# Performance work log

Hardware: AMD Instinct MI355X
Metric: run time of the kernel (lower is better)

The kernel has to match this reference:

```python
import jax, jax.numpy as jnp
import numpy as np

GROUP_SIZE = 128
LORA_SCALING = 32.0 / 16.0  # lora_alpha / r


def _unpack_rows(q):
    # q: int32 [n, m] -> uint4 values [n*8, m], 8 nibbles per int32 along axis 0
    shifts = (jnp.arange(8, dtype=jnp.int32) * 4)
    vals = (q[:, None, :] >> shifts[None, :, None]) & 0xF
    return vals.reshape(q.shape[0] * 8, q.shape[1])


def _unpack_cols(q):
    # q: int32 [g, m] -> uint4 values [g, m*8], 8 nibbles per int32 along axis 1
    shifts = (jnp.arange(8, dtype=jnp.int32) * 4)
    vals = (q[:, :, None] >> shifts[None, None, :]) & 0xF
    return vals.reshape(q.shape[0], q.shape[1] * 8)


def setup_inputs() -> dict:
    key = jax.random.key(0)
    ks = jax.random.split(key, 6)
    in_f, out_f, tokens, r = 4096, 11008, 64, 16
    g = in_f // GROUP_SIZE  # 32 groups
    x = jax.random.normal(ks[0], (tokens, in_f), dtype=jnp.float32)
    qweight = jax.random.randint(ks[1], (in_f // 8, out_f), jnp.iinfo(jnp.int32).min, jnp.iinfo(jnp.int32).max, dtype=jnp.int32)
    qzeros = jax.random.randint(ks[2], (g, out_f // 8), jnp.iinfo(jnp.int32).min, jnp.iinfo(jnp.int32).max, dtype=jnp.int32)
    scales = jax.random.uniform(ks[3], (g, out_f), dtype=jnp.float32) * 0.01 + 0.001
    lora_A = jax.random.normal(ks[4], (r, in_f), dtype=jnp.float32) * 0.02
    lora_B = jax.random.normal(ks[5], (out_f, r), dtype=jnp.float32) * 0.02
    return {"x": x, "qweight": qweight, "qzeros": qzeros, "scales": scales,
            "lora_A": lora_A, "lora_B": lora_B}


def reference(x, qweight, qzeros, scales, lora_A, lora_B):
    in_f = qweight.shape[0] * 8
    # --- GPTQ int4 dequant ---
    wq = _unpack_rows(qweight).astype(jnp.float32)          # [in, out]
    zeros = (_unpack_cols(qzeros) + 1).astype(jnp.float32)  # [groups, out] (GPTQ +1 offset)
    g_idx = jnp.arange(in_f) // GROUP_SIZE                  # [in]
    W = scales[g_idx] * (wq - zeros[g_idx])                 # [in, out]
    # base quantized matmul
    result = x @ W                                          # [tokens, out]
    # --- LoRA adapter (single active adapter, dropout=0, tmp_weight=1) ---
    lora_out = (x @ lora_A.T) @ lora_B.T                    # [tokens, out]
    return result + lora_out * LORA_SCALING
```

## Files before the change

kernel.cpp:

```cpp
#include <hip/hip_runtime.h>
#include <stdint.h>

#define TOKENS 64
#define IN_F   4096
#define OUT_F  11008
#define RANK   16
#define GS     128
#define NG     32
#define ZCOLS  (OUT_F / 8)
#define LORA_SCALE 2.0f

using short8  = __attribute__((ext_vector_type(8))) short;
using float4v = __attribute__((ext_vector_type(4))) float;

static __device__ inline uint16_t f2bf(float f, float* back) {
    uint32_t u = __float_as_uint(f);
    uint32_t r = (u + 0x7FFFu + ((u >> 16) & 1u)) >> 16;
    *back = __uint_as_float(r << 16);
    return (uint16_t)r;
}

__global__ __launch_bounds__(256) void prep_kernel(
        const float* __restrict__ x,
        const float* __restrict__ loraA,
        uint4* __restrict__ xf4,
        float* __restrict__ xsumT,
        float* __restrict__ midT) {
    __shared__ float redg[256];
    __shared__ float redm[4][16];
    const int t    = blockIdx.x;
    const int tid  = threadIdx.x;
    const int lane = tid & 63;
    const int wv   = tid >> 6;

    float4 xv[4];
    const float4* xp = (const float4*)(x + (size_t)t * IN_F + tid * 16);
    #pragma unroll
    for (int i = 0; i < 4; ++i) xv[i] = xp[i];

    union { uint16_t u[16]; uint4 q[2]; } ob;
    float s = 0.f;
    #pragma unroll
    for (int i = 0; i < 4; ++i) {
        float b;
        ob.u[i * 4 + 0] = f2bf(xv[i].x, &b); s += b;
        ob.u[i * 4 + 1] = f2bf(xv[i].y, &b); s += b;
        ob.u[i * 4 + 2] = f2bf(xv[i].z, &b); s += b;
        ob.u[i * 4 + 3] = f2bf(xv[i].w, &b); s += b;
    }
    {
        const int mm = t >> 4, nn = t & 15;
        const int kchunk = tid >> 1;
        #pragma unroll
        for (int i = 0; i < 2; ++i) {
            const int qd = (tid * 2 + i) & 3;
            xf4[(size_t)((mm * 128 + kchunk) * 64 + qd * 16 + nn)] = ob.q[i];
        }
    }
    redg[tid] = s;

    float pj[16];
    #pragma unroll
    for (int j = 0; j < 16; ++j) {
        const float4* ap = (const float4*)(loraA + (size_t)j * IN_F + tid * 16);
        float ps = 0.f;
        #pragma unroll
        for (int i = 0; i < 4; ++i) {
            float4 a = ap[i];
            ps += a.x * xv[i].x + a.y * xv[i].y + a.z * xv[i].z + a.w * xv[i].w;
        }
        pj[j] = ps;
    }
    #pragma unroll
    for (int j = 0; j < 16; ++j) {
        #pragma unroll
        for (int off = 32; off; off >>= 1) pj[j] += __shfl_down(pj[j], off);
    }
    if (lane == 0) {
        #pragma unroll
        for (int j = 0; j < 16; ++j) redm[wv][j] = pj[j];
    }
    __syncthreads();
    if (tid < NG) {
        float g = 0.f;
        #pragma unroll
        for (int i = 0; i < 8; ++i) g += redg[tid * 8 + i];
        xsumT[tid * TOKENS + t] = g;
    }
    if (tid < 16)
        midT[tid * TOKENS + t] = redm[0][tid] + redm[1][tid] + redm[2][tid] + redm[3][tid];
}

__global__ __launch_bounds__(256) void lora_out_kernel(
        const float* __restrict__ midT,
        const float* __restrict__ loraB,
        float* __restrict__ out) {
    const int gid = blockIdx.x * 256 + threadIdx.x;
    const int t = gid / OUT_F;
    const int o = gid - t * OUT_F;
    const float4* b4 = (const float4*)(loraB + (size_t)o * RANK);
    float s = 0.f;
    #pragma unroll
    for (int i = 0; i < 4; ++i) {
        float4 b = b4[i];
        s += b.x * midT[(i * 4 + 0) * TOKENS + t];
        s += b.y * midT[(i * 4 + 1) * TOKENS + t];
        s += b.z * midT[(i * 4 + 2) * TOKENS + t];
        s += b.w * midT[(i * 4 + 3) * TOKENS + t];
    }
    out[gid] = s * LORA_SCALE;
}

#define LOADG(st, g) do {                                                       \
    _Pragma("unroll")                                                           \
    for (int mt = 0; mt < 2; ++mt)                                              \
        _Pragma("unroll")                                                       \
        for (int ks = 0; ks < 4; ++ks)                                          \
            A[st][mt * 4 + ks] =                                                \
                xf4[(size_t)(((mh * 2 + mt) * 128 + (g) * 4 + ks) * 64) + lane];\
    _Pragma("unroll")                                                           \
    for (int ks = 0; ks < 4; ++ks)                                              \
        _Pragma("unroll")                                                       \
        for (int nh = 0; nh < 2; ++nh)                                          \
            B[st][ks * 2 + nh] =                                                \
                qwc[(size_t)((g) * 16 + ks * 4 + quad) * OUT_F + nh * 16];      \
    _Pragma("unroll")                                                           \
    for (int mt = 0; mt < 2; ++mt)                                              \
        XS[st][mt] = *(const float4*)(xsumT + (g) * 64 +                        \
                                      (mh * 2 + mt) * 16 + quad * 4);           \
    _Pragma("unroll")                                                           \
    for (int nh = 0; nh < 2; ++nh) {                                            \
        S[st][nh] = scales[(size_t)(g) * OUT_F + col0 + nh * 16 + n];           \
        Z[st][nh] = qz[(size_t)(g) * ZCOLS + ((col0 + nh * 16 + n) >> 3)];      \
    }                                                                           \
} while (0)

#define COMPUTEG(st) do {                                                       \
    float4v accg[2][2];                                                         \
    _Pragma("unroll")                                                           \
    for (int mt = 0; mt < 2; ++mt)                                              \
        _Pragma("unroll")                                                       \
        for (int nh = 0; nh < 2; ++nh)                                          \
            accg[mt][nh] = (float4v){0.f, 0.f, 0.f, 0.f};                       \
    _Pragma("unroll")                                                           \
    for (int ks = 0; ks < 4; ++ks) {                                            \
        union { uint4 u; short8 s; } af0, af1;                                  \
        af0.u = A[st][ks];                                                      \
        af1.u = A[st][4 + ks];                                                  \
        _Pragma("unroll")                                                       \
        for (int nh = 0; nh < 2; ++nh) {                                        \
            uint32_t q  = B[st][ks * 2 + nh];                                   \
            uint32_t lo = q & 0x0F0F0F0Fu;                                      \
            uint32_t hi = (q >> 4) & 0x0F0F0F0Fu;                               \
            union { uint32_t u32[4]; short8 s8; } bf;                           \
            _Pragma("unroll")                                                   \
            for (int i = 0; i < 4; ++i)                                         \
                bf.u32[i] = __builtin_amdgcn_perm(hi, lo,                       \
                                0x0C040C00u + i * 0x00010001u) | 0x43004300u;   \
            accg[0][nh] = __builtin_amdgcn_mfma_f32_16x16x32_bf16(af0.s, bf.s8, \
                                                            accg[0][nh], 0, 0, 0);\
            accg[1][nh] = __builtin_amdgcn_mfma_f32_16x16x32_bf16(af1.s, bf.s8, \
                                                            accg[1][nh], 0, 0, 0);\
        }                                                                       \
    }                                                                           \
    _Pragma("unroll")                                                           \
    for (int nh = 0; nh < 2; ++nh) {                                            \
        const float zoff = (float)(((Z[st][nh] >>                               \
                        (((col0 + nh * 16 + n) & 7) * 4)) & 0xFu) + 129u);      \
        const float scl = S[st][nh];                                            \
        _Pragma("unroll")                                                       \
        for (int mt = 0; mt < 2; ++mt) {                                        \
            const float xr[4] = {XS[st][mt].x, XS[st][mt].y,                    \
                                 XS[st][mt].z, XS[st][mt].w};                   \
            _Pragma("unroll")                                                   \
            for (int r = 0; r < 4; ++r)                                         \
                acc[mt][nh][r] = fmaf(scl, fmaf(-zoff, xr[r],                   \
                                      accg[mt][nh][r]), acc[mt][nh][r]);        \
        }                                                                       \
    }                                                                           \
} while (0)

__global__ __launch_bounds__(256, 3) void main_kernel(
        const uint32_t* __restrict__ qw,
        const uint32_t* __restrict__ qz,
        const float* __restrict__ scales,
        const uint4* __restrict__ xf4,
        const float* __restrict__ xsumT,
        float* __restrict__ out) {
    const int tid  = threadIdx.x;
    const int wv   = tid >> 6;
    const int lane = tid & 63;
    const int n    = lane & 15;
    const int quad = lane >> 4;
    const int mh   = wv & 1;
    const int cs   = wv >> 1;
    const int colblk = blockIdx.x >> 2;
    const int kseg   = blockIdx.x & 3;
    const int col0   = colblk * 64 + cs * 32;
    const int g0     = kseg * 8;

    const uint32_t* qwc = qw + col0 + n;

    float4v acc[2][2];
    #pragma unroll
    for (int mt = 0; mt < 2; ++mt)
        #pragma unroll
        for (int nh = 0; nh < 2; ++nh)
            acc[mt][nh] = (float4v){0.f, 0.f, 0.f, 0.f};

    uint4    A[2][8];
    uint32_t B[2][8];
    float4   XS[2][2];
    float    S[2][2];
    uint32_t Z[2][2];

    LOADG(0, g0);
    LOADG(1, g0 + 1);
    #pragma unroll
    for (int gi = 0; gi < 8; ++gi) {
        const int st = gi & 1;
        COMPUTEG(st);
        int gl = gi + 2; if (gl > 7) gl = 7;
        LOADG(st, g0 + gl);
    }

    #pragma unroll
    for (int mt = 0; mt < 2; ++mt)
        #pragma unroll
        for (int nh = 0; nh < 2; ++nh)
            #pragma unroll
            for (int r = 0; r < 4; ++r) {
                const int t = (mh * 2 + mt) * 16 + quad * 4 + r;
                atomicAdd(out + (size_t)t * OUT_F + col0 + nh * 16 + n,
                          acc[mt][nh][r]);
            }
}

extern "C" void kernel_launch(void* const* d_in, const int* in_sizes, int n_in,
                              void* d_out, int out_size, void* d_ws, size_t ws_size,
                              hipStream_t stream) {
    const float*    x      = (const float*)d_in[0];
    const uint32_t* qw     = (const uint32_t*)d_in[1];
    const uint32_t* qz     = (const uint32_t*)d_in[2];
    const float*    scales = (const float*)d_in[3];
    const float*    loraA  = (const float*)d_in[4];
    const float*    loraB  = (const float*)d_in[5];
    float* out = (float*)d_out;

    uint4* xf4   = (uint4*)d_ws;
    float* xsumT = (float*)((char*)d_ws + (size_t)TOKENS * IN_F * 2);
    float* midT  = xsumT + NG * TOKENS;

    prep_kernel<<<TOKENS, 256, 0, stream>>>(x, loraA, xf4, xsumT, midT);
    lora_out_kernel<<<(TOKENS * OUT_F) / 256, 256, 0, stream>>>(midT, loraB, out);
    main_kernel<<<(OUT_F / 64) * 4, 256, 0, stream>>>(qw, qz, scales, xf4, xsumT, out);
}
```

Baseline: 106.9 us.

## Fuse LoRA output into main GEMM and drop split-K atomics

```diff
diff --git a/kernel.cpp b/kernel.cpp
--- a/kernel.cpp
+++ b/kernel.cpp
@@ -20,12 +20,16 @@
     return (uint16_t)r;
 }
 
+static __device__ inline float dot4(float4 a, float4 b) {
+    return a.x * b.x + a.y * b.y + a.z * b.z + a.w * b.w;
+}
+
 __global__ __launch_bounds__(256) void prep_kernel(
         const float* __restrict__ x,
         const float* __restrict__ loraA,
         uint4* __restrict__ xf4,
         float* __restrict__ xsumT,
-        float* __restrict__ midT) {
+        float* __restrict__ midTT) {
     __shared__ float redg[256];
     __shared__ float redm[4][16];
     const int t    = blockIdx.x;
@@ -88,27 +92,7 @@
         xsumT[tid * TOKENS + t] = g;
     }
     if (tid < 16)
-        midT[tid * TOKENS + t] = redm[0][tid] + redm[1][tid] + redm[2][tid] + redm[3][tid];
-}
-
-__global__ __launch_bounds__(256) void lora_out_kernel(
-        const float* __restrict__ midT,
-        const float* __restrict__ loraB,
-        float* __restrict__ out) {
-    const int gid = blockIdx.x * 256 + threadIdx.x;
-    const int t = gid / OUT_F;
-    const int o = gid - t * OUT_F;
-    const float4* b4 = (const float4*)(loraB + (size_t)o * RANK);
-    float s = 0.f;
-    #pragma unroll
-    for (int i = 0; i < 4; ++i) {
-        float4 b = b4[i];
-        s += b.x * midT[(i * 4 + 0) * TOKENS + t];
-        s += b.y * midT[(i * 4 + 1) * TOKENS + t];
-        s += b.z * midT[(i * 4 + 2) * TOKENS + t];
-        s += b.w * midT[(i * 4 + 3) * TOKENS + t];
-    }
-    out[gid] = s * LORA_SCALE;
+        midTT[t * RANK + tid] = redm[0][tid] + redm[1][tid] + redm[2][tid] + redm[3][tid];
 }
 
 #define LOADG(st, g) do {                                                       \
@@ -120,72 +104,60 @@
                 xf4[(size_t)(((mh * 2 + mt) * 128 + (g) * 4 + ks) * 64) + lane];\
     _Pragma("unroll")                                                           \
     for (int ks = 0; ks < 4; ++ks)                                              \
-        _Pragma("unroll")                                                       \
-        for (int nh = 0; nh < 2; ++nh)                                          \
-            B[st][ks * 2 + nh] =                                                \
-                qwc[(size_t)((g) * 16 + ks * 4 + quad) * OUT_F + nh * 16];      \
+        B[st][ks] = qwc[(size_t)((g) * 16 + ks * 4 + quad) * OUT_F];            \
     _Pragma("unroll")                                                           \
     for (int mt = 0; mt < 2; ++mt)                                              \
         XS[st][mt] = *(const float4*)(xsumT + (g) * 64 +                        \
                                       (mh * 2 + mt) * 16 + quad * 4);           \
-    _Pragma("unroll")                                                           \
-    for (int nh = 0; nh < 2; ++nh) {                                            \
-        S[st][nh] = scales[(size_t)(g) * OUT_F + col0 + nh * 16 + n];           \
-        Z[st][nh] = qz[(size_t)(g) * ZCOLS + ((col0 + nh * 16 + n) >> 3)];      \
-    }                                                                           \
+    S[st] = scales[(size_t)(g) * OUT_F + col];                                  \
+    Z[st] = qz[(size_t)(g) * ZCOLS + (col >> 3)];                               \
 } while (0)
 
 #define COMPUTEG(st) do {                                                       \
-    float4v accg[2][2];                                                         \
-    _Pragma("unroll")                                                           \
-    for (int mt = 0; mt < 2; ++mt)                                              \
-        _Pragma("unroll")                                                       \
-        for (int nh = 0; nh < 2; ++nh)                                          \
-            accg[mt][nh] = (float4v){0.f, 0.f, 0.f, 0.f};                       \
+    float4v accg[2];                                                            \
+    accg[0] = (float4v){0.f, 0.f, 0.f, 0.f};                                    \
+    accg[1] = (float4v){0.f, 0.f, 0.f, 0.f};                                    \
     _Pragma("unroll")                                                           \
     for (int ks = 0; ks < 4; ++ks) {                                            \
         union { uint4 u; short8 s; } af0, af1;                                  \
         af0.u = A[st][ks];                                                      \
         af1.u = A[st][4 + ks];                                                  \
+        uint32_t q  = B[st][ks];                                                \
+        uint32_t lo = q & 0x0F0F0F0Fu;                                          \
+        uint32_t hi = (q >> 4) & 0x0F0F0F0Fu;                                   \
+        union { uint32_t u32[4]; short8 s8; } bf;                               \
         _Pragma("unroll")                                                       \
-        for (int nh = 0; nh < 2; ++nh) {                                        \
-            uint32_t q  = B[st][ks * 2 + nh];                                   \
-            uint32_t lo = q & 0x0F0F0F0Fu;                                      \
-            uint32_t hi = (q >> 4) & 0x0F0F0F0Fu;                               \
-            union { uint32_t u32[4]; short8 s8; } bf;                           \
-            _Pragma("unroll")                                                   \
-            for (int i = 0; i < 4; ++i)                                         \
-                bf.u32[i] = __builtin_amdgcn_perm(hi, lo,                       \
-                                0x0C040C00u + i * 0x00010001u) | 0x43004300u;   \
-            accg[0][nh] = __builtin_amdgcn_mfma_f32_16x16x32_bf16(af0.s, bf.s8, \
-                                                            accg[0][nh], 0, 0, 0);\
-            accg[1][nh] = __builtin_amdgcn_mfma_f32_16x16x32_bf16(af1.s, bf.s8, \
-                                                            accg[1][nh], 0, 0, 0);\
-        }                                                                       \
+        for (int i = 0; i < 4; ++i)                                             \
+            bf.u32[i] = __builtin_amdgcn_perm(hi, lo,                           \
+                            0x0C040C00u + i * 0x00010001u) | 0x43004300u;       \
+        accg[0] = __builtin_amdgcn_mfma_f32_16x16x32_bf16(af0.s, bf.s8,         \
+                                                          accg[0], 0, 0, 0);    \
+        accg[1] = __builtin_amdgcn_mfma_f32_16x16x32_bf16(af1.s, bf.s8,         \
+                                                          accg[1], 0, 0, 0);    \
     }                                                                           \
-    _Pragma("unroll")                                                           \
-    for (int nh = 0; nh < 2; ++nh) {                                            \
-        const float zoff = (float)(((Z[st][nh] >>                               \
-                        (((col0 + nh * 16 + n) & 7) * 4)) & 0xFu) + 129u);      \
-        const float scl = S[st][nh];                                            \
+    {                                                                           \
+        const float zoff = (float)(((Z[st] >> ((col & 7) * 4)) & 0xFu) + 129u); \
+        const float scl = S[st];                                                \
         _Pragma("unroll")                                                       \
         for (int mt = 0; mt < 2; ++mt) {                                        \
             const float xr[4] = {XS[st][mt].x, XS[st][mt].y,                    \
                                  XS[st][mt].z, XS[st][mt].w};                   \
             _Pragma("unroll")                                                   \
             for (int r = 0; r < 4; ++r)                                         \
-                acc[mt][nh][r] = fmaf(scl, fmaf(-zoff, xr[r],                   \
-                                      accg[mt][nh][r]), acc[mt][nh][r]);        \
+                acc[mt][r] = fmaf(scl, fmaf(-zoff, xr[r],                       \
+                                  accg[mt][r]), acc[mt][r]);                    \
         }                                                                       \
     }                                                                           \
 } while (0)
 
-__global__ __launch_bounds__(256, 3) void main_kernel(
+__global__ __launch_bounds__(256) void main_kernel(
         const uint32_t* __restrict__ qw,
         const uint32_t* __restrict__ qz,
         const float* __restrict__ scales,
         const uint4* __restrict__ xf4,
         const float* __restrict__ xsumT,
+        const float* __restrict__ midTT,
+        const float* __restrict__ loraB,
         float* __restrict__ out) {
     const int tid  = threadIdx.x;
     const int wv   = tid >> 6;
@@ -194,46 +166,44 @@
     const int quad = lane >> 4;
     const int mh   = wv & 1;
     const int cs   = wv >> 1;
-    const int colblk = blockIdx.x >> 2;
-    const int kseg   = blockIdx.x & 3;
-    const int col0   = colblk * 64 + cs * 32;
-    const int g0     = kseg * 8;
-
-    const uint32_t* qwc = qw + col0 + n;
-
-    float4v acc[2][2];
-    #pragma unroll
-    for (int mt = 0; mt < 2; ++mt)
-        #pragma unroll
-        for (int nh = 0; nh < 2; ++nh)
-            acc[mt][nh] = (float4v){0.f, 0.f, 0.f, 0.f};
+    const int col  = blockIdx.x * 32 + cs * 16 + n;
+
+    const uint32_t* qwc = qw + col;
+
+    float4v acc[2];
+    acc[0] = (float4v){0.f, 0.f, 0.f, 0.f};
+    acc[1] = (float4v){0.f, 0.f, 0.f, 0.f};
 
     uint4    A[2][8];
-    uint32_t B[2][8];
+    uint32_t B[2][4];
     float4   XS[2][2];
-    float    S[2][2];
-    uint32_t Z[2][2];
-
-    LOADG(0, g0);
-    LOADG(1, g0 + 1);
-    #pragma unroll
-    for (int gi = 0; gi < 8; ++gi) {
-        const int st = gi & 1;
+    float    S[2];
+    uint32_t Z[2];
+
+    LOADG(0, 0);
+    LOADG(1, 1);
+    #pragma unroll 2
+    for (int g = 0; g < NG - 2; ++g) {
+        const int st = g & 1;
         COMPUTEG(st);
-        int gl = gi + 2; if (gl > 7) gl = 7;
-        LOADG(st, g0 + gl);
-    }
-
-    #pragma unroll
-    for (int mt = 0; mt < 2; ++mt)
-        #pragma unroll
-        for (int nh = 0; nh < 2; ++nh)
-            #pragma unroll
-            for (int r = 0; r < 4; ++r) {
-                const int t = (mh * 2 + mt) * 16 + quad * 4 + r;
-                atomicAdd(out + (size_t)t * OUT_F + col0 + nh * 16 + n,
-                          acc[mt][nh][r]);
-            }
+        LOADG(st, g + 2);
+    }
+    COMPUTEG((NG - 2) & 1);
+    COMPUTEG((NG - 1) & 1);
+
+    const float4* b4 = (const float4*)(loraB + (size_t)col * RANK);
+    const float4 b0 = b4[0], b1 = b4[1], b2 = b4[2], b3 = b4[3];
+    #pragma unroll
+    for (int mt = 0; mt < 2; ++mt) {
+        #pragma unroll
+        for (int r = 0; r < 4; ++r) {
+            const int t = (mh * 2 + mt) * 16 + quad * 4 + r;
+            const float4* m4 = (const float4*)(midTT + t * RANK);
+            const float l = dot4(b0, m4[0]) + dot4(b1, m4[1]) +
+                            dot4(b2, m4[2]) + dot4(b3, m4[3]);
+            out[(size_t)t * OUT_F + col] = acc[mt][r] + LORA_SCALE * l;
+        }
+    }
 }
 
 extern "C" void kernel_launch(void* const* d_in, const int* in_sizes, int n_in,
@@ -249,9 +219,9 @@
 
     uint4* xf4   = (uint4*)d_ws;
     float* xsumT = (float*)((char*)d_ws + (size_t)TOKENS * IN_F * 2);
-    float* midT  = xsumT + NG * TOKENS;
-
-    prep_kernel<<<TOKENS, 256, 0, stream>>>(x, loraA, xf4, xsumT, midT);
-    lora_out_kernel<<<(TOKENS * OUT_F) / 256, 256, 0, stream>>>(midT, loraB, out);
-    main_kernel<<<(OUT_F / 64) * 4, 256, 0, stream>>>(qw, qz, scales, xf4, xsumT, out);
-}
+    float* midTT = xsumT + NG * TOKENS;
+
+    prep_kernel<<<TOKENS, 256, 0, stream>>>(x, loraA, xf4, xsumT, midTT);
+    main_kernel<<<OUT_F / 32, 256, 0, stream>>>(qw, qz, scales, xf4, xsumT,
+                                                midTT, loraB, out);
+}
```

New measurement: 113.4 us. +6.1%, slower.

## Stage quantized weights through LDS with direct global-to-LDS double-buffered loads

Applied to the files above, without the earlier changes.

```diff
diff --git a/kernel.cpp b/kernel.cpp
--- a/kernel.cpp
+++ b/kernel.cpp
@@ -12,6 +12,9 @@
 
 using short8  = __attribute__((ext_vector_type(8))) short;
 using float4v = __attribute__((ext_vector_type(4))) float;
+
+typedef __attribute__((address_space(3))) uint32_t       lds_u32_t;
+typedef __attribute__((address_space(1))) const uint32_t glb_u32_t;
 
 static __device__ inline uint16_t f2bf(float f, float* back) {
     uint32_t u = __float_as_uint(f);
@@ -111,82 +114,14 @@
     out[gid] = s * LORA_SCALE;
 }
 
-#define LOADG(st, g) do {                                                       \
-    _Pragma("unroll")                                                           \
-    for (int mt = 0; mt < 2; ++mt)                                              \
-        _Pragma("unroll")                                                       \
-        for (int ks = 0; ks < 4; ++ks)                                          \
-            A[st][mt * 4 + ks] =                                                \
-                xf4[(size_t)(((mh * 2 + mt) * 128 + (g) * 4 + ks) * 64) + lane];\
-    _Pragma("unroll")                                                           \
-    for (int ks = 0; ks < 4; ++ks)                                              \
-        _Pragma("unroll")                                                       \
-        for (int nh = 0; nh < 2; ++nh)                                          \
-            B[st][ks * 2 + nh] =                                                \
-                qwc[(size_t)((g) * 16 + ks * 4 + quad) * OUT_F + nh * 16];      \
-    _Pragma("unroll")                                                           \
-    for (int mt = 0; mt < 2; ++mt)                                              \
-        XS[st][mt] = *(const float4*)(xsumT + (g) * 64 +                        \
-                                      (mh * 2 + mt) * 16 + quad * 4);           \
-    _Pragma("unroll")                                                           \
-    for (int nh = 0; nh < 2; ++nh) {                                            \
-        S[st][nh] = scales[(size_t)(g) * OUT_F + col0 + nh * 16 + n];           \
-        Z[st][nh] = qz[(size_t)(g) * ZCOLS + ((col0 + nh * 16 + n) >> 3)];      \
-    }                                                                           \
-} while (0)
-
-#define COMPUTEG(st) do {                                                       \
-    float4v accg[2][2];                                                         \
-    _Pragma("unroll")                                                           \
-    for (int mt = 0; mt < 2; ++mt)                                              \
-        _Pragma("unroll")                                                       \
-        for (int nh = 0; nh < 2; ++nh)                                          \
-            accg[mt][nh] = (float4v){0.f, 0.f, 0.f, 0.f};                       \
-    _Pragma("unroll")                                                           \
-    for (int ks = 0; ks < 4; ++ks) {                                            \
-        union { uint4 u; short8 s; } af0, af1;                                  \
-        af0.u = A[st][ks];                                                      \
-        af1.u = A[st][4 + ks];                                                  \
-        _Pragma("unroll")                                                       \
-        for (int nh = 0; nh < 2; ++nh) {                                        \
-            uint32_t q  = B[st][ks * 2 + nh];                                   \
-            uint32_t lo = q & 0x0F0F0F0Fu;                                      \
-            uint32_t hi = (q >> 4) & 0x0F0F0F0Fu;                               \
-            union { uint32_t u32[4]; short8 s8; } bf;                           \
-            _Pragma("unroll")                                                   \
-            for (int i = 0; i < 4; ++i)                                         \
-                bf.u32[i] = __builtin_amdgcn_perm(hi, lo,                       \
-                                0x0C040C00u + i * 0x00010001u) | 0x43004300u;   \
-            accg[0][nh] = __builtin_amdgcn_mfma_f32_16x16x32_bf16(af0.s, bf.s8, \
-                                                            accg[0][nh], 0, 0, 0);\
-            accg[1][nh] = __builtin_amdgcn_mfma_f32_16x16x32_bf16(af1.s, bf.s8, \
-                                                            accg[1][nh], 0, 0, 0);\
-        }                                                                       \
-    }                                                                           \
-    _Pragma("unroll")                                                           \
-    for (int nh = 0; nh < 2; ++nh) {                                            \
-        const float zoff = (float)(((Z[st][nh] >>                               \
-                        (((col0 + nh * 16 + n) & 7) * 4)) & 0xFu) + 129u);      \
-        const float scl = S[st][nh];                                            \
-        _Pragma("unroll")                                                       \
-        for (int mt = 0; mt < 2; ++mt) {                                        \
-            const float xr[4] = {XS[st][mt].x, XS[st][mt].y,                    \
-                                 XS[st][mt].z, XS[st][mt].w};                   \
-            _Pragma("unroll")                                                   \
-            for (int r = 0; r < 4; ++r)                                         \
-                acc[mt][nh][r] = fmaf(scl, fmaf(-zoff, xr[r],                   \
-                                      accg[mt][nh][r]), acc[mt][nh][r]);        \
-        }                                                                       \
-    }                                                                           \
-} while (0)
-
-__global__ __launch_bounds__(256, 3) void main_kernel(
+__global__ __launch_bounds__(256, 2) void main_kernel(
         const uint32_t* __restrict__ qw,
         const uint32_t* __restrict__ qz,
         const float* __restrict__ scales,
         const uint4* __restrict__ xf4,
         const float* __restrict__ xsumT,
         float* __restrict__ out) {
+    __shared__ uint32_t bq[2][16 * 64];
     const int tid  = threadIdx.x;
     const int wv   = tid >> 6;
     const int lane = tid & 63;
@@ -196,10 +131,13 @@
     const int cs   = wv >> 1;
     const int colblk = blockIdx.x >> 2;
     const int kseg   = blockIdx.x & 3;
-    const int col0   = colblk * 64 + cs * 32;
-    const int g0     = kseg * 8;
-
-    const uint32_t* qwc = qw + col0 + n;
+    const int blkcol0 = colblk * 64;
+    const int col0    = blkcol0 + cs * 32;
+    const int g0      = kseg * 8;
+
+    const uint32_t* qsrc = qw + (size_t)(g0 * 16 + (tid >> 4)) * OUT_F
+                              + blkcol0 + (tid & 15) * 4;
+    const size_t gstride = (size_t)16 * OUT_F;
 
     float4v acc[2][2];
     #pragma unroll
@@ -208,20 +146,89 @@
         for (int nh = 0; nh < 2; ++nh)
             acc[mt][nh] = (float4v){0.f, 0.f, 0.f, 0.f};
 
-    uint4    A[2][8];
-    uint32_t B[2][8];
-    float4   XS[2][2];
-    float    S[2][2];
-    uint32_t Z[2][2];
-
-    LOADG(0, g0);
-    LOADG(1, g0 + 1);
+    __builtin_amdgcn_global_load_lds((glb_u32_t*)qsrc,
+                                     (lds_u32_t*)&bq[0][wv * 256], 16, 0, 0);
+    __syncthreads();
+
     #pragma unroll
     for (int gi = 0; gi < 8; ++gi) {
-        const int st = gi & 1;
-        COMPUTEG(st);
-        int gl = gi + 2; if (gl > 7) gl = 7;
-        LOADG(st, g0 + gl);
+        const int cur = gi & 1;
+        const int g   = g0 + gi;
+
+        uint4 A[8];
+        #pragma unroll
+        for (int mt = 0; mt < 2; ++mt)
+            #pragma unroll
+            for (int ks = 0; ks < 4; ++ks)
+                A[mt * 4 + ks] =
+                    xf4[(size_t)(((mh * 2 + mt) * 128 + g * 4 + ks) * 64) + lane];
+        float4 XS[2];
+        #pragma unroll
+        for (int mt = 0; mt < 2; ++mt)
+            XS[mt] = *(const float4*)(xsumT + g * 64 + (mh * 2 + mt) * 16 + quad * 4);
+        float S[2]; uint32_t Z[2];
+        #pragma unroll
+        for (int nh = 0; nh < 2; ++nh) {
+            S[nh] = scales[(size_t)g * OUT_F + col0 + nh * 16 + n];
+            Z[nh] = qz[(size_t)g * ZCOLS + ((col0 + nh * 16 + n) >> 3)];
+        }
+
+        if (gi < 7)
+            __builtin_amdgcn_global_load_lds(
+                (glb_u32_t*)(qsrc + (size_t)(gi + 1) * gstride),
+                (lds_u32_t*)&bq[cur ^ 1][wv * 256], 16, 0, 0);
+
+        uint32_t Bw[8];
+        #pragma unroll
+        for (int ks = 0; ks < 4; ++ks)
+            #pragma unroll
+            for (int nh = 0; nh < 2; ++nh)
+                Bw[ks * 2 + nh] =
+                    bq[cur][(ks * 4 + quad) * 64 + cs * 32 + nh * 16 + n];
+
+        float4v accg[2][2];
+        #pragma unroll
+        for (int mt = 0; mt < 2; ++mt)
+            #pragma unroll
+            for (int nh = 0; nh < 2; ++nh)
+                accg[mt][nh] = (float4v){0.f, 0.f, 0.f, 0.f};
+        #pragma unroll
+        for (int ks = 0; ks < 4; ++ks) {
+            union { uint4 u; short8 s; } af0, af1;
+            af0.u = A[ks];
+            af1.u = A[4 + ks];
+            #pragma unroll
+            for (int nh = 0; nh < 2; ++nh) {
+                uint32_t q  = Bw[ks * 2 + nh];
+                uint32_t lo = q & 0x0F0F0F0Fu;
+                uint32_t hi = (q >> 4) & 0x0F0F0F0Fu;
+                union { uint32_t u32[4]; short8 s8; } bf;
+                #pragma unroll
+                for (int i = 0; i < 4; ++i)
+                    bf.u32[i] = __builtin_amdgcn_perm(hi, lo,
+                                    0x0C040C00u + i * 0x00010001u) | 0x43004300u;
+                accg[0][nh] = __builtin_amdgcn_mfma_f32_16x16x32_bf16(
+                                    af0.s, bf.s8, accg[0][nh], 0, 0, 0);
+                accg[1][nh] = __builtin_amdgcn_mfma_f32_16x16x32_bf16(
+                                    af1.s, bf.s8, accg[1][nh], 0, 0, 0);
+            }
+        }
+        #pragma unroll
+        for (int nh = 0; nh < 2; ++nh) {
+            const float zoff =
+                (float)(((Z[nh] >> (((col0 + nh * 16 + n) & 7) * 4)) & 0xFu) + 129u);
+            const float scl = S[nh];
+            #pragma unroll
+            for (int mt = 0; mt < 2; ++mt) {
+                const float xr[4] = {XS[mt].x, XS[mt].y, XS[mt].z, XS[mt].w};
+                #pragma unroll
+                for (int r = 0; r < 4; ++r)
+                    acc[mt][nh][r] = fmaf(scl, fmaf(-zoff, xr[r], accg[mt][nh][r]),
+                                          acc[mt][nh][r]);
+            }
+        }
+
+        __syncthreads();
     }
 
     #pragma unroll
```

New measurement: 113.6 us. 6.3% more time.
